# Kernel optimization log

Hardware: AMD Instinct MI355X
Metric: run time of the kernel (lower is better)

## Reference

```python
import jax, jax.numpy as jnp
import numpy as np

N_EMBED = 1024
N_HEADS = 16
HEAD_DIM = N_EMBED // N_HEADS


def setup_inputs() -> dict:
    key = jax.random.key(0)
    ks = jax.random.split(key, 5)
    x = jax.random.normal(ks[0], (4, 2048, N_EMBED), dtype=jnp.float32)
    # Linear params stored as [in, out] (y = x @ W + b), math-equivalent to torch Linear
    scale_attn = 1.0 / np.sqrt(N_EMBED)
    W_attn = jax.random.normal(ks[1], (N_EMBED, 3 * N_EMBED), dtype=jnp.float32) * scale_attn
    b_attn = jax.random.normal(ks[2], (3 * N_EMBED,), dtype=jnp.float32) * 0.02
    W_proj = jax.random.normal(ks[3], (N_EMBED, N_EMBED), dtype=jnp.float32) * scale_attn
    b_proj = jax.random.normal(ks[4], (N_EMBED,), dtype=jnp.float32) * 0.02
    return {"x": x, "W_attn": W_attn, "b_attn": b_attn, "W_proj": W_proj, "b_proj": b_proj}


def reference(x, W_attn, b_attn, W_proj, b_proj):
    BS, SL, ED = x.shape
    qkv = x @ W_attn + b_attn                      # [B, S, 3E]
    q, k, v = jnp.split(qkv, 3, axis=2)
    # [B, H, S, D]
    def heads(t):
        return t.reshape(BS, SL, N_HEADS, HEAD_DIM).transpose(0, 2, 1, 3)
    q, k, v = heads(q), heads(k), heads(v)
    att = jnp.einsum('bhqd,bhkd->bhqk', q, k) * (HEAD_DIM ** -0.5)
    causal = jnp.tril(jnp.ones((SL, SL), dtype=bool))
    att = jnp.where(causal[None, None], att, -jnp.inf)
    att = jax.nn.softmax(att, axis=-1)
    y = jnp.einsum('bhqk,bhkd->bhqd', att, v)      # [B, H, S, D]
    y = y.transpose(0, 2, 1, 3).reshape(BS, SL, ED)
    return y @ W_proj + b_proj
```

## Files before the change

kernel.cpp:

```cpp
#include <hip/hip_runtime.h>


#define BATCH 4
#define SEQ   2048
#define EMB   1024
#define NH    16
#define HD    64

typedef __bf16 bf16;
typedef __bf16 bf16x8 __attribute__((ext_vector_type(8)));
typedef __bf16 bf16x4 __attribute__((ext_vector_type(4)));
typedef float  f32x4  __attribute__((ext_vector_type(4)));

__device__ __forceinline__ void ld_lds16(const void* g, void* l) {
  __builtin_amdgcn_global_load_lds(
      (const __attribute__((address_space(1))) void*)g,
      (__attribute__((address_space(3))) void*)l, 16, 0, 0);
}

__global__ void prep(const float* __restrict__ x, bf16* __restrict__ xb, int n,
                     const float* __restrict__ Wa, const float* __restrict__ Wp,
                     bf16* __restrict__ WaT, bf16* __restrict__ WpT) {
  __shared__ float tile[32][33];
  int bid = blockIdx.x;
  if (bid < 8192) {
    int i = (bid * 256 + threadIdx.x) * 4;
    if (i + 3 < n) {
      float4 v = *(const float4*)(x + i);
      bf16 o0 = (bf16)v.x, o1 = (bf16)v.y, o2 = (bf16)v.z, o3 = (bf16)v.w;
      xb[i] = o0; xb[i+1] = o1; xb[i+2] = o2; xb[i+3] = o3;
    }
    return;
  }
  int tb = bid - 8192;
  int bx = tb & 127;
  int byk = tb >> 7;
  const float* W; bf16* WT; int N;
  if (bx < 96) { W = Wa; WT = WaT; N = 3072; }
  else         { W = Wp; WT = WpT; N = 1024; bx -= 96; }
  int n0 = bx * 32, k0 = byk * 32;
  int tx = threadIdx.x & 31, ty = threadIdx.x >> 5;
#pragma unroll
  for (int r = 0; r < 4; r++) {
    int k = k0 + ty + r * 8;
    tile[ty + r * 8][tx] = W[(long)k * N + n0 + tx];
  }
  __syncthreads();
#pragma unroll
  for (int r = 0; r < 4; r++) {
    int nn = n0 + ty + r * 8;
    WT[(long)nn * EMB + k0 + tx] = (bf16)tile[tx][ty + r * 8];
  }
}

#define QSCALE 0.18033688f

__global__ __launch_bounds__(256, 2) void gemm8p(
    const bf16* __restrict__ A, const bf16* __restrict__ Bt,
    const float* __restrict__ bias,
    bf16* __restrict__ q, bf16* __restrict__ k, bf16* __restrict__ v)
{
  __shared__ __align__(16) bf16 lds[24576];
  int lin = blockIdx.x;
  int xcd = lin & 7, s = lin >> 3;
  int by = xcd * 8 + (s & 7);
  int bx = s >> 3;
  int m0 = by * 128, n0 = bx * 256;
  int t = threadIdx.x;
  int wid = t >> 6, lane = t & 63;
  int l15 = lane & 15, quad = lane >> 4;
  int wc = wid;

  const bf16* Ag = A + (long)m0 * EMB;
  const bf16* Bg = Bt + (long)n0 * EMB;

  f32x4 acc[8][4] = {};
  bf16x8 af[8], bfr[4];
  constexpr int NT = EMB / 32;
  int ph8 = ((quad + (l15 >> 1)) & 3) * 8;

#define LDSA(b) (lds + (b) * 4096)
#define LDSB(b) (lds + 8192 + (b) * 8192)

#define ISSUE64(gbase, rowoff, ldst, ktt)                                      \
  { int r_ = (rowoff) + (t >> 2);                                              \
    int g_ = ((t & 3) - ((t >> 3) & 3)) & 3;                                   \
    ld_lds16(&(gbase)[(long)r_ * EMB + (ktt) + g_ * 8],                        \
             (ldst) + ((rowoff) + wid * 16) * 32); }

#define RD_A(mi) { int r_ = (mi) * 16 + l15;                                   \
    af[mi] = *(const bf16x8*)&Ab[r_ * 32 + ph8]; }
#define RD_B(ni) { int r_ = wc * 64 + (ni) * 16 + l15;                         \
    bfr[ni] = *(const bf16x8*)&Bb[r_ * 32 + ph8]; }

#define FENCE asm volatile("" ::: "memory")
#define BAR   { FENCE; __builtin_amdgcn_s_barrier(); FENCE; }

#define MFMAC(nlo)                                                             \
  { __builtin_amdgcn_s_setprio(1);                                             \
    _Pragma("unroll") for (int mi_ = 0; mi_ < 8; ++mi_)                        \
      _Pragma("unroll") for (int nj_ = 0; nj_ < 2; ++nj_)                      \
        acc[mi_][(nlo) + nj_] = __builtin_amdgcn_mfma_f32_16x16x32_bf16(       \
            af[mi_], bfr[(nlo) + nj_], acc[mi_][(nlo) + nj_], 0, 0, 0);        \
    __builtin_amdgcn_s_setprio(0); }

  ISSUE64(Ag, 0,   LDSA(0), 0);
  ISSUE64(Ag, 64,  LDSA(0), 0);
  ISSUE64(Bg, 0,   LDSB(0), 0);
  ISSUE64(Bg, 64,  LDSB(0), 0);
  ISSUE64(Bg, 128, LDSB(0), 0);
  ISSUE64(Bg, 192, LDSB(0), 0);
  ISSUE64(Ag, 0,   LDSA(1), 32);
  asm volatile("s_waitcnt vmcnt(1)" ::: "memory");
  BAR;

#pragma unroll 2
  for (int tt = 0; tt < NT; ++tt) {
    const bf16* Ab = LDSA(tt & 1);
    const bf16* Bb = LDSB(tt & 1);
    bf16* An = LDSA((tt + 1) & 1);
    bf16* Bn = LDSB((tt + 1) & 1);
    bf16* Ac = LDSA(tt & 1);
    int kn  = (tt + 1 < NT ? tt + 1 : NT - 1) * 32;
    int kn2 = (tt + 2 < NT ? tt + 2 : NT - 1) * 32;

#pragma unroll
    for (int mi = 0; mi < 8; ++mi) RD_A(mi);
    RD_B(0); RD_B(1);
    ISSUE64(Ag, 64,  An, kn);
    ISSUE64(Bg, 0,   Bn, kn);
    ISSUE64(Bg, 64,  Bn, kn);
    ISSUE64(Bg, 128, Bn, kn);
    BAR; MFMAC(0); BAR;
    RD_B(2); RD_B(3);
    ISSUE64(Bg, 192, Bn, kn);
    ISSUE64(Ag, 0,   Ac, kn2);
    asm volatile("s_waitcnt vmcnt(1)" ::: "memory");
    BAR; MFMAC(2); BAR;
  }

  asm volatile("s_waitcnt vmcnt(0)" ::: "memory");
  __syncthreads();

  int which = bx >> 2;
  if (which < 2) {
    bf16* dst = (which == 0) ? q : k;
    float scale = (which == 0) ? QSCALE : 1.0f;
#pragma unroll
    for (int mi = 0; mi < 8; ++mi)
#pragma unroll
      for (int ni = 0; ni < 4; ++ni) {
        int gcol = n0 + wc * 64 + ni * 16 + l15;
        float bv = bias[gcol];
        int e = gcol & 1023, h = e >> 6, d = e & 63;
#pragma unroll
        for (int i = 0; i < 4; ++i) {
          int grow = m0 + mi * 16 + quad * 4 + i;
          int b = grow >> 11, ss = grow & 2047;
          dst[(((long)b * NH + h) * SEQ + ss) * HD + d] =
              (bf16)((acc[mi][ni][i] + bv) * scale);
        }
      }
  } else {
#pragma unroll
    for (int mi = 0; mi < 8; ++mi)
#pragma unroll
      for (int ni = 0; ni < 4; ++ni) {
        int gcol = n0 + wc * 64 + ni * 16 + l15;
        float bv = bias[gcol];
        int e = gcol & 1023, h = e >> 6, d = e & 63;
#pragma unroll
        for (int i = 0; i < 4; ++i) {
          int grow = m0 + mi * 16 + quad * 4 + i;
          int b = grow >> 11, ss = grow & 2047;
          v[(((long)b * NH + h) * HD + d) * SEQ + ss] =
              (bf16)(acc[mi][ni][i] + bv);
        }
      }
  }
#undef LDSA
#undef LDSB
#undef ISSUE64
#undef RD_A
#undef RD_B
#undef MFMAC
}

__global__ __launch_bounds__(256, 3) void gemm_proj(
    const bf16* __restrict__ A, const bf16* __restrict__ Bt,
    const float* __restrict__ bias, float* __restrict__ out)
{
  __shared__ __align__(16) bf16 Al[128 * 64];
  __shared__ __align__(16) bf16 Bl[64 * 64];
  int lin = blockIdx.x;
  int xcd = lin & 7, s = lin >> 3;
  int bx = s >> 3, by = xcd * 8 + (s & 7);
  int m0 = by * 128;
  int n0 = bx * 64;
  int t = threadIdx.x;
  int wave = t >> 6, lane = t & 63;
  int l15 = lane & 15, quad = lane >> 4;
  int wm = (wave & 1) * 64, wn = (wave >> 1) * 32;

  f32x4 acc[4][2] = {};

  for (int kt = 0; kt < EMB; kt += 64) {
    __syncthreads();
#pragma unroll
    for (int it = 0; it < 4; ++it) {
      int c = it * 256 + t;
      int row = c >> 3, u = c & 7;
      ld_lds16(&A[(long)(m0 + row) * EMB + kt + ((u ^ (row & 7)) * 8)],
               &Al[(it * 256 + wave * 64) * 8]);
    }
    {
      int c = t;
      int row = c >> 3, u = c & 7;
      ld_lds16(&Bt[(long)(n0 + row) * EMB + kt + ((u ^ (row & 7)) * 8)],
               &Bl[(wave * 64) * 8]);
      c = 256 + t;
      row = c >> 3; u = c & 7;
      ld_lds16(&Bt[(long)(n0 + row) * EMB + kt + ((u ^ (row & 7)) * 8)],
               &Bl[(256 + wave * 64) * 8]);
    }
    __syncthreads();
#pragma unroll
    for (int ks = 0; ks < 2; ++ks) {
      bf16x8 af[4], bfr[2];
#pragma unroll
      for (int i = 0; i < 4; ++i) {
        int r = wm + i * 16 + l15;
        af[i] = *(const bf16x8*)(&Al[r * 64 + (((ks * 4 + quad) ^ (r & 7)) * 8)]);
      }
#pragma unroll
      for (int i = 0; i < 2; ++i) {
        int r = wn + i * 16 + l15;
        bfr[i] = *(const bf16x8*)(&Bl[r * 64 + (((ks * 4 + quad) ^ (r & 7)) * 8)]);
      }
#pragma unroll
      for (int mi = 0; mi < 4; ++mi)
#pragma unroll
        for (int ni = 0; ni < 2; ++ni)
          acc[mi][ni] = __builtin_amdgcn_mfma_f32_16x16x32_bf16(af[mi], bfr[ni], acc[mi][ni], 0, 0, 0);
    }
  }

#pragma unroll
  for (int mi = 0; mi < 4; ++mi)
#pragma unroll
    for (int ni = 0; ni < 2; ++ni) {
      int gcol = n0 + wn + ni * 16 + l15;
      float bv = bias[gcol];
#pragma unroll
      for (int i = 0; i < 4; ++i) {
        int grow = m0 + wm + mi * 16 + quad * 4 + i;
        out[(long)grow * EMB + gcol] = acc[mi][ni][i] + bv;
      }
    }
}

__global__ __launch_bounds__(256, 2) void attn(
    const bf16* __restrict__ Q, const bf16* __restrict__ K,
    const bf16* __restrict__ Vt, bf16* __restrict__ Y)
{
  __shared__ __align__(16) bf16 Kl[64 * 64];
  __shared__ __align__(16) bf16 Vl[64 * 64];
  int L = blockIdx.x;
  int a = L >> 3;
  int hd = (L & 7) + 8 * (a & 7);
  int st = a >> 3;
  int b = hd >> 4, h = hd & 15;
  const bf16* Qp  = Q  + (((long)b * NH + h) * SEQ) * HD;
  const bf16* Kp  = K  + (((long)b * NH + h) * SEQ) * HD;
  const bf16* Vtp = Vt + (((long)b * NH + h) * HD) * SEQ;
  int t = threadIdx.x, wave = t >> 6, lane = t & 63;
  int l15 = lane & 15, quad = lane >> 4;
  int rkbase = ((l15 >> 2) << 3) + (l15 & 3);

#pragma unroll 1
  for (int pass = 0; pass < 2; ++pass) {
    int q0 = (pass == 0) ? st * 128 : (SEQ - 128) - st * 128;
    int wq0 = q0 + wave * 32;

    bf16x8 qf[2][2];
#pragma unroll
    for (int m = 0; m < 2; ++m) {
      const bf16* qrow = Qp + (long)(wq0 + m * 16 + l15) * HD + quad * 8;
      qf[m][0] = *(const bf16x8*)(qrow);
      qf[m][1] = *(const bf16x8*)(qrow + 32);
    }
    float lrow[2] = {};
    f32x4 oacc[2][4] = {};

    int ntiles = q0 / 64 + 2;
#pragma unroll 1
    for (int kt = 0; kt < ntiles; ++kt) {
      int k0 = kt * 64;
      __syncthreads();
#pragma unroll
      for (int it = 0; it < 2; ++it) {
        int cu = it * 256 + t;
        int row = cu >> 3, u = cu & 7;
        ld_lds16(&Kp[(long)(k0 + row) * HD + ((u ^ (row & 7)) * 8)],
                 &Kl[(it * 256 + wave * 64) * 8]);
        ld_lds16(&Vtp[(long)row * SEQ + k0 + ((u ^ (row & 7)) * 8)],
                 &Vl[(it * 256 + wave * 64) * 8]);
      }
      __syncthreads();
      if (k0 > wq0 + 31) continue;

      f32x4 sc[2][4] = {};
#pragma unroll
      for (int kd = 0; kd < 2; ++kd) {
#pragma unroll
        for (int f = 0; f < 4; ++f) {
          int rk = ((f >> 1) << 5) + ((f & 1) << 2) + rkbase;
          bf16x8 kf = *(const bf16x8*)(&Kl[rk * 64 + (((kd * 4 + quad) ^ (rk & 7)) * 8)]);
          sc[0][f] = __builtin_amdgcn_mfma_f32_16x16x32_bf16(kf, qf[0][kd], sc[0][f], 0, 0, 0);
          sc[1][f] = __builtin_amdgcn_mfma_f32_16x16x32_bf16(kf, qf[1][kd], sc[1][f], 0, 0, 0);
        }
      }

      bool full = (k0 + 63 <= wq0);
      bf16x8 pb[2][2];
#pragma unroll
      for (int m = 0; m < 2; ++m) {
        int qr = wq0 + m * 16 + l15;
#pragma unroll
        for (int f = 0; f < 4; ++f) {
          int kgb = k0 + ((f >> 1) << 5) + quad * 8 + ((f & 1) << 2);
          float e[4];
#pragma unroll
          for (int i = 0; i < 4; ++i) {
            float x = sc[m][f][i];
            if (!full) x = (kgb + i <= qr) ? x : -1e30f;
            e[i] = __builtin_amdgcn_exp2f(x);
          }
          lrow[m] += (e[0] + e[1]) + (e[2] + e[3]);
#pragma unroll
          for (int i = 0; i < 4; ++i)
            pb[m][f >> 1][((f & 1) << 2) + i] = (bf16)e[i];
        }
      }

#pragma unroll
      for (int kp = 0; kp < 2; ++kp) {
#pragma unroll
        for (int ni = 0; ni < 4; ++ni) {
          int dd = ni * 16 + l15;
          bf16x8 vf = *(const bf16x8*)(&Vl[dd * 64 + (((kp * 4 + quad) ^ (dd & 7)) * 8)]);
          oacc[0][ni] = __builtin_amdgcn_mfma_f32_16x16x32_bf16(vf, pb[0][kp], oacc[0][ni], 0, 0, 0);
          oacc[1][ni] = __builtin_amdgcn_mfma_f32_16x16x32_bf16(vf, pb[1][kp], oacc[1][ni], 0, 0, 0);
        }
      }
    }
#pragma unroll
    for (int m = 0; m < 2; ++m) {
      float rs = lrow[m];
      rs += __shfl_xor(rs, 16);
      rs += __shfl_xor(rs, 32);
      float inv = 1.0f / rs;
      int qr = wq0 + m * 16 + l15;
      bf16* dst = Y + ((long)(b * SEQ + qr)) * EMB + h * HD + quad * 4;
#pragma unroll
      for (int ni = 0; ni < 4; ++ni) {
        bf16x4 o;
#pragma unroll
        for (int i = 0; i < 4; ++i) o[i] = (bf16)(oacc[m][ni][i] * inv);
        *(bf16x4*)(&dst[ni * 16]) = o;
      }
    }
  }
}

extern "C" void kernel_launch(void* const* d_in, const int* in_sizes, int n_in,
                              void* d_out, int out_size, void* d_ws, size_t ws_size,
                              hipStream_t stream) {
  const float* x      = (const float*)d_in[0];
  const float* W_attn = (const float*)d_in[1];
  const float* b_attn = (const float*)d_in[2];
  const float* W_proj = (const float*)d_in[3];
  const float* b_proj = (const float*)d_in[4];
  float* out = (float*)d_out;
  char* ws = (char*)d_ws;
  bf16* xb  = (bf16*)(ws);
  bf16* WaT = (bf16*)(ws + 16777216);
  bf16* WpT = (bf16*)(ws + 23068672);
  bf16* Qb  = (bf16*)(ws + 25165824);
  bf16* Kb  = (bf16*)(ws + 41943040);
  bf16* Vtb = (bf16*)(ws + 58720256);
  bf16* Yb  = (bf16*)(ws + 75497472);

  prep<<<12288, 256, 0, stream>>>(x, xb, BATCH * SEQ * EMB,
                                  W_attn, W_proj, WaT, WpT);
  gemm8p<<<768, 256, 0, stream>>>(xb, WaT, b_attn, Qb, Kb, Vtb);
  attn<<<512, 256, 0, stream>>>(Qb, Kb, Vtb, Yb);
  gemm_proj<<<1024, 256, 0, stream>>>(Yb, WpT, b_proj, out);
}
```

Before: 232.8 us.

## Template pipelined GEMM and reuse it for the output projection

Turns the QKV GEMM into a template over N-fragment count and output mode, and replaces the simpler gemm_proj with an instance using 128x128 tiles and the double-buffered direct-to-LDS pipeline. The main-loop schedule also changes: all B loads are issued up front and the two MFMA halves are split by a single barrier instead of four. The intent is to give the projection the better-pipelined loop and to cut barrier stalls in both GEMMs. In exchange the projection launches fewer blocks (512 instead of 1024) and the fewer barriers could add LDS hazards or reduce overlap.

After: 236.4 us. No clear change (+1.5%).

```diff
diff --git a/kernel.cpp b/kernel.cpp
--- a/kernel.cpp
+++ b/kernel.cpp
@@ -55,17 +55,22 @@
 
 #define QSCALE 0.18033688f
 
-__global__ __launch_bounds__(256, 2) void gemm8p(
+template <int NF, int MODE>
+__global__ __launch_bounds__(256, 2) void gemm_cv(
     const bf16* __restrict__ A, const bf16* __restrict__ Bt,
     const float* __restrict__ bias,
-    bf16* __restrict__ q, bf16* __restrict__ k, bf16* __restrict__ v)
+    bf16* __restrict__ q, bf16* __restrict__ k, bf16* __restrict__ v,
+    float* __restrict__ out)
 {
-  __shared__ __align__(16) bf16 lds[24576];
+  constexpr int BN = NF * 64;
+  constexpr int WN = NF * 16;
+  constexpr int BELEM = BN * 32;
+  __shared__ __align__(16) bf16 lds[8192 + 2 * BELEM];
   int lin = blockIdx.x;
   int xcd = lin & 7, s = lin >> 3;
   int by = xcd * 8 + (s & 7);
   int bx = s >> 3;
-  int m0 = by * 128, n0 = bx * 256;
+  int m0 = by * 128, n0 = bx * BN;
   int t = threadIdx.x;
   int wid = t >> 6, lane = t & 63;
   int l15 = lane & 15, quad = lane >> 4;
@@ -74,13 +79,13 @@
   const bf16* Ag = A + (long)m0 * EMB;
   const bf16* Bg = Bt + (long)n0 * EMB;
 
-  f32x4 acc[8][4] = {};
-  bf16x8 af[8], bfr[4];
+  f32x4 acc[8][NF] = {};
+  bf16x8 af[8], bfr[NF];
   constexpr int NT = EMB / 32;
   int ph8 = ((quad + (l15 >> 1)) & 3) * 8;
 
 #define LDSA(b) (lds + (b) * 4096)
-#define LDSB(b) (lds + 8192 + (b) * 8192)
+#define LDSB(b) (lds + 8192 + (b) * BELEM)
 
 #define ISSUE64(gbase, rowoff, ldst, ktt)                                      \
   { int r_ = (rowoff) + (t >> 2);                                              \
@@ -90,27 +95,25 @@
 
 #define RD_A(mi) { int r_ = (mi) * 16 + l15;                                   \
     af[mi] = *(const bf16x8*)&Ab[r_ * 32 + ph8]; }
-#define RD_B(ni) { int r_ = wc * 64 + (ni) * 16 + l15;                         \
+#define RD_B(ni) { int r_ = wc * WN + (ni) * 16 + l15;                         \
     bfr[ni] = *(const bf16x8*)&Bb[r_ * 32 + ph8]; }
 
 #define FENCE asm volatile("" ::: "memory")
 #define BAR   { FENCE; __builtin_amdgcn_s_barrier(); FENCE; }
 
-#define MFMAC(nlo)                                                             \
+#define MFMAH(nlo, nhi)                                                        \
   { __builtin_amdgcn_s_setprio(1);                                             \
     _Pragma("unroll") for (int mi_ = 0; mi_ < 8; ++mi_)                        \
-      _Pragma("unroll") for (int nj_ = 0; nj_ < 2; ++nj_)                      \
-        acc[mi_][(nlo) + nj_] = __builtin_amdgcn_mfma_f32_16x16x32_bf16(       \
-            af[mi_], bfr[(nlo) + nj_], acc[mi_][(nlo) + nj_], 0, 0, 0);        \
+      _Pragma("unroll") for (int nj_ = (nlo); nj_ < (nhi); ++nj_)              \
+        acc[mi_][nj_] = __builtin_amdgcn_mfma_f32_16x16x32_bf16(               \
+            af[mi_], bfr[nj_], acc[mi_][nj_], 0, 0, 0);                        \
     __builtin_amdgcn_s_setprio(0); }
 
-  ISSUE64(Ag, 0,   LDSA(0), 0);
-  ISSUE64(Ag, 64,  LDSA(0), 0);
-  ISSUE64(Bg, 0,   LDSB(0), 0);
-  ISSUE64(Bg, 64,  LDSB(0), 0);
-  ISSUE64(Bg, 128, LDSB(0), 0);
-  ISSUE64(Bg, 192, LDSB(0), 0);
-  ISSUE64(Ag, 0,   LDSA(1), 32);
+  ISSUE64(Ag, 0,  LDSA(0), 0);
+  ISSUE64(Ag, 64, LDSA(0), 0);
+#pragma unroll
+  for (int u = 0; u < NF; ++u) ISSUE64(Bg, u * 64, LDSB(0), 0);
+  ISSUE64(Ag, 0, LDSA(1), 32);
   asm volatile("s_waitcnt vmcnt(1)" ::: "memory");
   BAR;
 
@@ -126,137 +129,79 @@
 
 #pragma unroll
     for (int mi = 0; mi < 8; ++mi) RD_A(mi);
-    RD_B(0); RD_B(1);
-    ISSUE64(Ag, 64,  An, kn);
-    ISSUE64(Bg, 0,   Bn, kn);
-    ISSUE64(Bg, 64,  Bn, kn);
-    ISSUE64(Bg, 128, Bn, kn);
-    BAR; MFMAC(0); BAR;
-    RD_B(2); RD_B(3);
-    ISSUE64(Bg, 192, Bn, kn);
-    ISSUE64(Ag, 0,   Ac, kn2);
+#pragma unroll
+    for (int ni = 0; ni < NF; ++ni) RD_B(ni);
+    ISSUE64(Ag, 64, An, kn);
+#pragma unroll
+    for (int u = 0; u < NF; ++u) ISSUE64(Bg, u * 64, Bn, kn);
+    MFMAH(0, NF / 2);
+    BAR;
+    ISSUE64(Ag, 0, Ac, kn2);
+    MFMAH(NF / 2, NF);
     asm volatile("s_waitcnt vmcnt(1)" ::: "memory");
-    BAR; MFMAC(2); BAR;
+    BAR;
   }
 
   asm volatile("s_waitcnt vmcnt(0)" ::: "memory");
   __syncthreads();
 
-  int which = bx >> 2;
-  if (which < 2) {
-    bf16* dst = (which == 0) ? q : k;
-    float scale = (which == 0) ? QSCALE : 1.0f;
+  if (MODE == 1) {
 #pragma unroll
     for (int mi = 0; mi < 8; ++mi)
 #pragma unroll
-      for (int ni = 0; ni < 4; ++ni) {
-        int gcol = n0 + wc * 64 + ni * 16 + l15;
+      for (int ni = 0; ni < NF; ++ni) {
+        int gcol = n0 + wc * WN + ni * 16 + l15;
         float bv = bias[gcol];
-        int e = gcol & 1023, h = e >> 6, d = e & 63;
 #pragma unroll
         for (int i = 0; i < 4; ++i) {
           int grow = m0 + mi * 16 + quad * 4 + i;
-          int b = grow >> 11, ss = grow & 2047;
-          dst[(((long)b * NH + h) * SEQ + ss) * HD + d] =
-              (bf16)((acc[mi][ni][i] + bv) * scale);
+          out[(long)grow * EMB + gcol] = acc[mi][ni][i] + bv;
         }
       }
   } else {
-#pragma unroll
-    for (int mi = 0; mi < 8; ++mi)
-#pragma unroll
-      for (int ni = 0; ni < 4; ++ni) {
-        int gcol = n0 + wc * 64 + ni * 16 + l15;
-        float bv = bias[gcol];
-        int e = gcol & 1023, h = e >> 6, d = e & 63;
-#pragma unroll
-        for (int i = 0; i < 4; ++i) {
-          int grow = m0 + mi * 16 + quad * 4 + i;
-          int b = grow >> 11, ss = grow & 2047;
-          v[(((long)b * NH + h) * HD + d) * SEQ + ss] =
-              (bf16)(acc[mi][ni][i] + bv);
-        }
-      }
+    int which = bx >> 2;
+    if (which < 2) {
+      bf16* dst = (which == 0) ? q : k;
+      float scale = (which == 0) ? QSCALE : 1.0f;
+#pragma unroll
+      for (int mi = 0; mi < 8; ++mi)
+#pragma unroll
+        for (int ni = 0; ni < NF; ++ni) {
+          int gcol = n0 + wc * WN + ni * 16 + l15;
+          float bv = bias[gcol];
+          int e = gcol & 1023, h = e >> 6, d = e & 63;
+#pragma unroll
+          for (int i = 0; i < 4; ++i) {
+            int grow = m0 + mi * 16 + quad * 4 + i;
+            int b = grow >> 11, ss = grow & 2047;
+            dst[(((long)b * NH + h) * SEQ + ss) * HD + d] =
+                (bf16)((acc[mi][ni][i] + bv) * scale);
+          }
+        }
+    } else {
+#pragma unroll
+      for (int mi = 0; mi < 8; ++mi)
+#pragma unroll
+        for (int ni = 0; ni < NF; ++ni) {
+          int gcol = n0 + wc * WN + ni * 16 + l15;
+          float bv = bias[gcol];
+          int e = gcol & 1023, h = e >> 6, d = e & 63;
+#pragma unroll
+          for (int i = 0; i < 4; ++i) {
+            int grow = m0 + mi * 16 + quad * 4 + i;
+            int b = grow >> 11, ss = grow & 2047;
+            v[(((long)b * NH + h) * HD + d) * SEQ + ss] =
+                (bf16)(acc[mi][ni][i] + bv);
+          }
+        }
+    }
   }
 #undef LDSA
 #undef LDSB
 #undef ISSUE64
 #undef RD_A
 #undef RD_B
-#undef MFMAC
-}
-
-__global__ __launch_bounds__(256, 3) void gemm_proj(
-    const bf16* __restrict__ A, const bf16* __restrict__ Bt,
-    const float* __restrict__ bias, float* __restrict__ out)
-{
-  __shared__ __align__(16) bf16 Al[128 * 64];
-  __shared__ __align__(16) bf16 Bl[64 * 64];
-  int lin = blockIdx.x;
-  int xcd = lin & 7, s = lin >> 3;
-  int bx = s >> 3, by = xcd * 8 + (s & 7);
-  int m0 = by * 128;
-  int n0 = bx * 64;
-  int t = threadIdx.x;
-  int wave = t >> 6, lane = t & 63;
-  int l15 = lane & 15, quad = lane >> 4;
-  int wm = (wave & 1) * 64, wn = (wave >> 1) * 32;
-
-  f32x4 acc[4][2] = {};
-
-  for (int kt = 0; kt < EMB; kt += 64) {
-    __syncthreads();
-#pragma unroll
-    for (int it = 0; it < 4; ++it) {
-      int c = it * 256 + t;
-      int row = c >> 3, u = c & 7;
-      ld_lds16(&A[(long)(m0 + row) * EMB + kt + ((u ^ (row & 7)) * 8)],
-               &Al[(it * 256 + wave * 64) * 8]);
-    }
-    {
-      int c = t;
-      int row = c >> 3, u = c & 7;
-      ld_lds16(&Bt[(long)(n0 + row) * EMB + kt + ((u ^ (row & 7)) * 8)],
-               &Bl[(wave * 64) * 8]);
-      c = 256 + t;
-      row = c >> 3; u = c & 7;
-      ld_lds16(&Bt[(long)(n0 + row) * EMB + kt + ((u ^ (row & 7)) * 8)],
-               &Bl[(256 + wave * 64) * 8]);
-    }
-    __syncthreads();
-#pragma unroll
-    for (int ks = 0; ks < 2; ++ks) {
-      bf16x8 af[4], bfr[2];
-#pragma unroll
-      for (int i = 0; i < 4; ++i) {
-        int r = wm + i * 16 + l15;
-        af[i] = *(const bf16x8*)(&Al[r * 64 + (((ks * 4 + quad) ^ (r & 7)) * 8)]);
-      }
-#pragma unroll
-      for (int i = 0; i < 2; ++i) {
-        int r = wn + i * 16 + l15;
-        bfr[i] = *(const bf16x8*)(&Bl[r * 64 + (((ks * 4 + quad) ^ (r & 7)) * 8)]);
-      }
-#pragma unroll
-      for (int mi = 0; mi < 4; ++mi)
-#pragma unroll
-        for (int ni = 0; ni < 2; ++ni)
-          acc[mi][ni] = __builtin_amdgcn_mfma_f32_16x16x32_bf16(af[mi], bfr[ni], acc[mi][ni], 0, 0, 0);
-    }
-  }
-
-#pragma unroll
-  for (int mi = 0; mi < 4; ++mi)
-#pragma unroll
-    for (int ni = 0; ni < 2; ++ni) {
-      int gcol = n0 + wn + ni * 16 + l15;
-      float bv = bias[gcol];
-#pragma unroll
-      for (int i = 0; i < 4; ++i) {
-        int grow = m0 + wm + mi * 16 + quad * 4 + i;
-        out[(long)grow * EMB + gcol] = acc[mi][ni][i] + bv;
-      }
-    }
+#undef MFMAH
 }
 
 __global__ __launch_bounds__(256, 2) void attn(
@@ -393,7 +338,8 @@
 
   prep<<<12288, 256, 0, stream>>>(x, xb, BATCH * SEQ * EMB,
                                   W_attn, W_proj, WaT, WpT);
-  gemm8p<<<768, 256, 0, stream>>>(xb, WaT, b_attn, Qb, Kb, Vtb);
+  gemm_cv<4, 0><<<768, 256, 0, stream>>>(xb, WaT, b_attn, Qb, Kb, Vtb, nullptr);
   attn<<<512, 256, 0, stream>>>(Qb, Kb, Vtb, Yb);
-  gemm_proj<<<1024, 256, 0, stream>>>(Yb, WpT, b_proj, out);
-}
+  gemm_cv<2, 1><<<512, 256, 0, stream>>>(Yb, WpT, b_proj,
+                                         nullptr, nullptr, nullptr, out);
+}
```
